# Kernel optimization log

Measured on AMD Instinct MI355X. Metric: run time of the kernel, lower is better.

Reference implementation:

```python
import jax, jax.numpy as jnp
import numpy as np

NUM_GROUPS = 32
EPS = 1e-6


def group_norm(x, gamma, beta):
    b, c, h, w = x.shape
    xg = x.reshape(b, NUM_GROUPS, c // NUM_GROUPS, h, w)
    mean = jnp.mean(xg, axis=(2, 3, 4), keepdims=True)
    var = jnp.var(xg, axis=(2, 3, 4), keepdims=True)
    xg = (xg - mean) * jax.lax.rsqrt(var + EPS)
    x = xg.reshape(b, c, h, w)
    return x * gamma[None, :, None, None] + beta[None, :, None, None]


def conv1x1(x, w, b):
    # x: [B,C,H,W], w: [Cout,Cin], b: [Cout]
    return jnp.einsum('bchw,oc->bohw', x, w) + b[None, :, None, None]


def setup_inputs() -> dict:
    key = jax.random.key(0)
    ks = jax.random.split(key, 11)
    B, C, H, W = 2, 512, 64, 64
    s = 1.0 / np.sqrt(C)
    return {
        'x': jax.random.normal(ks[0], (B, C, H, W), jnp.float32),
        'norm_gamma': jnp.ones((C,), jnp.float32),
        'norm_beta': jnp.zeros((C,), jnp.float32),
        'wq': jax.random.normal(ks[1], (C, C), jnp.float32) * s,
        'bq': jnp.zeros((C,), jnp.float32),
        'wk': jax.random.normal(ks[2], (C, C), jnp.float32) * s,
        'bk': jnp.zeros((C,), jnp.float32),
        'wv': jax.random.normal(ks[3], (C, C), jnp.float32) * s,
        'bv': jnp.zeros((C,), jnp.float32),
        'wo': jax.random.normal(ks[4], (C, C), jnp.float32) * s,
        'bo': jnp.zeros((C,), jnp.float32),
    }


def reference(x, norm_gamma, norm_beta, wq, bq, wk, bk, wv, bv, wo, bo):
    b, c, h, w = x.shape
    hn = group_norm(x, norm_gamma, norm_beta)
    q = conv1x1(hn, wq, bq).reshape(b, c, h * w)  # [B,C,HW]
    k = conv1x1(hn, wk, bk).reshape(b, c, h * w)
    v = conv1x1(hn, wv, bv).reshape(b, c, h * w)
    scale = jnp.asarray(c, x.dtype) ** -0.5
    # scores[b,i,j] = sum_c q[b,c,i] * k[b,c,j]
    scores = jnp.einsum('bci,bcj->bij', q, k) * scale
    attn = jax.nn.softmax(scores, axis=2)
    # out[b,c,i] = sum_j v[b,c,j] * attn[b,i,j]
    out = jnp.einsum('bcj,bij->bci', v, attn).reshape(b, c, h, w)
    out = conv1x1(out, wo, bo)
    return x + out
```

## Files before the change

### kernel.cpp

```cpp
#include <hip/hip_runtime.h>
#include <hip/hip_bf16.h>

using u16 = unsigned short;
typedef __attribute__((ext_vector_type(4))) float f32x4;
typedef __attribute__((ext_vector_type(8))) __bf16 bf16x8;
typedef __attribute__((ext_vector_type(8))) short s16x8;
typedef __attribute__((ext_vector_type(4))) short s16x4;

#define DEVI __device__ __forceinline__

constexpr int BATCH = 2, C = 512, HW = 4096, NG = 32, CPG = 16;

DEVI float b2f(u16 u) { union { unsigned u; float f; } a; a.u = ((unsigned)u) << 16; return a.f; }
DEVI u16 f2b(float f) {
  union { float f; unsigned u; } a; a.f = f;
  unsigned r = a.u + 0x7fffu + ((a.u >> 16) & 1u);
  return (u16)(r >> 16);
}

DEVI void xcd_remap(int& bx, int& by, int& bz) {
  const int nx = gridDim.x, ny = gridDim.y;
  const int nwg = nx * ny * gridDim.z;
  const int flat = blockIdx.x + nx * (blockIdx.y + ny * blockIdx.z);
  const int cpx = nwg >> 3;
  const int w = (flat & 7) * cpx + (flat >> 3);
  bx = w % nx;
  const int t = w / nx;
  by = t % ny;
  bz = t / ny;
}

__global__ __launch_bounds__(256) void cvt_w(const float* __restrict__ a, const float* __restrict__ b,
                                             const float* __restrict__ c, const float* __restrict__ d,
                                             u16* __restrict__ out, float* __restrict__ stats) {
  if (blockIdx.x == 0 && threadIdx.x < 128) stats[threadIdx.x] = 0.f;
  int i = blockIdx.x * 256 + threadIdx.x;
  int w = i >> 16;
  int off = (i & 65535) * 4;
  const float* s = (w == 0) ? a : (w == 1) ? b : (w == 2) ? c : d;
  f32x4 v = *(const f32x4*)(s + off);
  s16x4 o;
  o[0] = (short)f2b(v[0]); o[1] = (short)f2b(v[1]); o[2] = (short)f2b(v[2]); o[3] = (short)f2b(v[3]);
  *(s16x4*)(out + (size_t)w * 262144 + off) = o;
}

__global__ __launch_bounds__(256) void gn_stats(const float* __restrict__ x, float* __restrict__ stats) {
  const int bg = blockIdx.x >> 3, part = blockIdx.x & 7;
  const f32x4* xg = (const f32x4*)(x + (size_t)bg * (CPG * HW)) + part * 2048;
  float s = 0.f, ss = 0.f;
  #pragma unroll
  for (int i = 0; i < 8; ++i) {
    f32x4 v = xg[i * 256 + threadIdx.x];
    s += v[0] + v[1] + v[2] + v[3];
    ss += v[0] * v[0] + v[1] * v[1] + v[2] * v[2] + v[3] * v[3];
  }
  #pragma unroll
  for (int o = 32; o; o >>= 1) { s += __shfl_xor(s, o); ss += __shfl_xor(ss, o); }
  if ((threadIdx.x & 63) == 0) {
    atomicAdd(&stats[bg * 2], s);
    atomicAdd(&stats[bg * 2 + 1], ss);
  }
}

__global__ __launch_bounds__(256) void gn_normT(const float* __restrict__ x, const float* __restrict__ stats,
                                                const float* __restrict__ gamma, const float* __restrict__ beta,
                                                u16* __restrict__ hnT) {
  __shared__ u16 tile[64][66];
  int b = blockIdx.z, c0 = blockIdx.y * 64, h0 = blockIdx.x * 64;
  int t = threadIdx.x;
  const float* xb = x + ((size_t)b * C + c0) * HW + h0;
  int r = t / 16, cc = (t % 16) * 4;
  const float inv = 1.f / (float)(CPG * HW);
  #pragma unroll
  for (int it = 0; it < 4; ++it) {
    int rr = it * 16 + r;
    int ch = c0 + rr;
    int g = b * NG + (ch >> 4);
    float S = stats[g * 2], SS = stats[g * 2 + 1];
    float mean = S * inv;
    float rstd = rsqrtf(SS * inv - mean * mean + 1e-6f);
    float ga = gamma[ch] * rstd;
    float be = beta[ch] - mean * ga;
    f32x4 v = *(const f32x4*)(xb + (size_t)rr * HW + cc);
    #pragma unroll
    for (int j = 0; j < 4; ++j) tile[rr][cc + j] = f2b(v[j] * ga + be);
  }
  __syncthreads();
  u16* op = hnT + (size_t)b * HW * C + (size_t)h0 * C + c0;
  int hr2 = t / 8, cg = (t % 8) * 8;
  #pragma unroll
  for (int it = 0; it < 2; ++it) {
    int hr = it * 32 + hr2;
    s16x8 o8;
    #pragma unroll
    for (int j = 0; j < 8; ++j) o8[j] = (short)tile[cg + j][hr];
    *(s16x8*)(op + (size_t)hr * C + cg) = o8;
  }
}

#define EPI_BIAS_M 1
#define EPI_BIAS_N 2
#define EPI_RESID  4
#define EPI_F32OUT 8
#define EPI_QK     32

template <int EPI>
__global__ __launch_bounds__(256) void gemm_bt(const u16* __restrict__ A, const u16* __restrict__ Bt,
                                               void* __restrict__ Co, int M, int N, int K,
                                               long long sA, long long sB, long long sC,
                                               const float* __restrict__ bias,
                                               const float* __restrict__ biasB,
                                               const float* __restrict__ resid, long long sR) {
  (void)M;
  __shared__ u16 ldsA[128 * 64];
  __shared__ u16 ldsB[128 * 64];
  const int tid = threadIdx.x;
  int bn, bm, bz;
  xcd_remap(bn, bm, bz);
  A += (size_t)bz * sA;
  Bt += (size_t)bz * sB;
  const int wave = tid >> 6, lane = tid & 63;
  const int wr = wave >> 1, wc = wave & 1;
  f32x4 acc[4][4] = {};

  const int srow = tid >> 3;
  const int sch = (tid & 7) ^ (srow & 7);
  const u16* gA = A + (size_t)(bm * 128 + srow) * K + sch * 8;
  const u16* gB = Bt + (size_t)(bn * 128 + srow) * K + sch * 8;
  u16* lA = ldsA + wave * 512;
  u16* lB = ldsB + wave * 512;

  for (int k0 = 0; k0 < K; k0 += 64) {
    #pragma unroll
    for (int cc = 0; cc < 4; ++cc) {
      __builtin_amdgcn_global_load_lds(
          (const __attribute__((address_space(1))) void*)(gA + (size_t)cc * 32 * K + k0),
          (__attribute__((address_space(3))) void*)(lA + cc * 2048), 16, 0, 0);
      __builtin_amdgcn_global_load_lds(
          (const __attribute__((address_space(1))) void*)(gB + (size_t)cc * 32 * K + k0),
          (__attribute__((address_space(3))) void*)(lB + cc * 2048), 16, 0, 0);
    }
    __syncthreads();
    #pragma unroll
    for (int kk = 0; kk < 2; ++kk) {
      bf16x8 af[4], bfv[4];
      #pragma unroll
      for (int m = 0; m < 4; ++m) {
        int r = wr * 64 + m * 16 + (lane & 15);
        int chunk = (kk * 4 + (lane >> 4)) ^ (r & 7);
        af[m] = *(const bf16x8*)(ldsA + r * 64 + chunk * 8);
      }
      #pragma unroll
      for (int n = 0; n < 4; ++n) {
        int r = wc * 64 + n * 16 + (lane & 15);
        int chunk = (kk * 4 + (lane >> 4)) ^ (r & 7);
        bfv[n] = *(const bf16x8*)(ldsB + r * 64 + chunk * 8);
      }
      #pragma unroll
      for (int m = 0; m < 4; ++m)
        #pragma unroll
        for (int n = 0; n < 4; ++n)
          acc[m][n] = __builtin_amdgcn_mfma_f32_16x16x32_bf16(af[m], bfv[n], acc[m][n], 0, 0, 0);
    }
    __syncthreads();
  }

  const int col0 = bn * 128 + wc * 64;
  const int row0 = bm * 128 + wr * 64 + ((lane >> 4) << 2);
  #pragma unroll
  for (int m = 0; m < 4; ++m) {
    #pragma unroll
    for (int j = 0; j < 4; ++j) {
      int gm = row0 + m * 16 + j;
      float bm_v = (EPI & EPI_BIAS_M) ? bias[gm] : 0.f;
      #pragma unroll
      for (int n = 0; n < 4; ++n) {
        int gn = col0 + n * 16 + (lane & 15);
        float v = acc[m][n][j] + bm_v;
        if (EPI & EPI_BIAS_N) {
          if (EPI & EPI_QK) v += (gn < 512) ? bias[gn] : biasB[gn - 512];
          else v += bias[gn];
        }
        if (EPI & EPI_RESID) v += resid[(size_t)bz * sR + (size_t)gm * N + gn];
        if (EPI & EPI_F32OUT)
          ((float*)Co)[(size_t)bz * sC + (size_t)gm * N + gn] = v;
        else
          ((u16*)Co)[(size_t)bz * sC + (size_t)gm * N + gn] = f2b(v);
      }
    }
  }
}

template <bool SCALED>
__global__ __launch_bounds__(512, 2) void gemm256(
    const u16* __restrict__ Ag, const u16* __restrict__ Bg,
    u16* __restrict__ Co, u16* __restrict__ Co2, int zSwitch,
    int Nld, int ldK, int nsplitLog, int kLen,
    long long sA, long long sB, long long sC, float scale) {
  __shared__ u16 lds[65536];
  const int tid = threadIdx.x;
  const int lane = tid & 63, w = tid >> 6;
  const int wm = w >> 2, wn = w & 3;
  const int l15 = lane & 15, l4 = lane >> 4;
  int bn, bm, z;
  xcd_remap(bn, bm, z);
  const int bz = z >> nsplitLog, kz = z & ((1 << nsplitLog) - 1);
  const int kStart = kz * kLen;
  const int NT = kLen >> 6;

  const int rStage = w * 8 + (lane >> 3);
  const int gch = (lane & 7) ^ (lane >> 3);
  const u16* gA = Ag + (size_t)bz * sA + (size_t)(bm * 256) * ldK + kStart + gch * 8;
  const u16* gB = Bg + (size_t)bz * sB + (size_t)(bn * 256) * ldK + kStart + gch * 8;

  f32x4 acc[8][4] = {};
  bf16x8 aF[4][2], bF[2][2][2];

  const int hB = wn >> 1, qB = wn & 1;
  const u16* pA0 = lds + (0 * 4 + wm) * 8192;
  const u16* pA1 = lds + (1 * 4 + wm) * 8192;
  const u16* pB0 = lds + (0 * 4 + 2 + hB) * 8192;
  const u16* pB1 = lds + (1 * 4 + 2 + hB) * 8192;

  #define STAGE(TT, DB, AB, HF) { \
    const u16* gbase = (AB) ? gB : gA; \
    u16* l0 = lds + ((DB) * 4 + (AB) * 2 + (HF)) * 8192 + w * 512; \
    _Pragma("unroll") for (int s = 0; s < 2; ++s) { \
      const u16* gp = gbase + (size_t)((HF) * 128 + s * 64 + rStage) * ldK + (TT) * 64; \
      __builtin_amdgcn_global_load_lds((const __attribute__((address_space(1))) void*)gp, \
          (__attribute__((address_space(3))) void*)(l0 + s * 4096), 16, 0, 0); } }

  #define LOAD_A(P, MH) { _Pragma("unroll") for (int j = 0; j < 4; ++j) \
    _Pragma("unroll") for (int kk = 0; kk < 2; ++kk) { \
      const int r_ = (MH) * 64 + j * 16 + l15; const int c_ = (kk * 4 + l4) ^ (r_ & 7); \
      aF[j][kk] = *(const bf16x8*)((P) + r_ * 64 + c_ * 8); } }

  #define LOAD_B(P, NH) { _Pragma("unroll") for (int j = 0; j < 2; ++j) \
    _Pragma("unroll") for (int kk = 0; kk < 2; ++kk) { \
      const int r_ = qB * 64 + (NH) * 32 + j * 16 + l15; const int c_ = (kk * 4 + l4) ^ (r_ & 7); \
      bF[NH][j][kk] = *(const bf16x8*)((P) + r_ * 64 + c_ * 8); } }

  #define MM(MH, NH) { __builtin_amdgcn_s_setprio(1); \
    _Pragma("unroll") for (int j = 0; j < 4; ++j) \
      _Pragma("unroll") for (int j2 = 0; j2 < 2; ++j2) \
        _Pragma("unroll") for (int kk = 0; kk < 2; ++kk) \
          acc[(MH) * 4 + j][(NH) * 2 + j2] = __builtin_amdgcn_mfma_f32_16x16x32_bf16( \
              aF[j][kk], bF[NH][j2][kk], acc[(MH) * 4 + j][(NH) * 2 + j2], 0, 0, 0); \
    __builtin_amdgcn_s_setprio(0); }

  #define BAR __builtin_amdgcn_s_barrier()
  #define WLG { asm volatile("s_waitcnt lgkmcnt(0)" ::: "memory"); __builtin_amdgcn_sched_barrier(0); }
  #define LG8 asm volatile("s_waitcnt lgkmcnt(8)" ::: "memory")
  #define WV4 asm volatile("s_waitcnt vmcnt(4)" ::: "memory")
  #define WV0 asm volatile("s_waitcnt vmcnt(0)" ::: "memory")

  STAGE(0, 0, 1, 0); STAGE(0, 0, 1, 1);
  STAGE(0, 0, 0, 0); STAGE(0, 0, 0, 1);
  STAGE(1, 1, 1, 0); STAGE(1, 1, 1, 1);
  WV4; BAR;

  const int NI = NT / 2 - 1;
  for (int i = 0; i < NI; ++i) {
    const int t1 = 2 * i + 1, u0 = 2 * i + 2, u1 = 2 * i + 3;
    LOAD_A(pA0, 0); LOAD_B(pB0, 0); STAGE(t1, 1, 0, 0); LG8; BAR; WLG; MM(0, 0); BAR;
    LOAD_B(pB0, 1); STAGE(t1, 1, 0, 1); BAR; WLG; MM(0, 1); BAR;
    LOAD_A(pA0, 1); STAGE(u0, 0, 1, 0); BAR; WLG; MM(1, 1); BAR;
    STAGE(u0, 0, 1, 1); BAR; WLG; MM(1, 0); WV4; BAR;
    LOAD_A(pA1, 0); LOAD_B(pB1, 0); STAGE(u0, 0, 0, 0); LG8; BAR; WLG; MM(0, 0); BAR;
    LOAD_B(pB1, 1); STAGE(u0, 0, 0, 1); BAR; WLG; MM(0, 1); BAR;
    LOAD_A(pA1, 1); STAGE(u1, 1, 1, 0); BAR; WLG; MM(1, 1); BAR;
    STAGE(u1, 1, 1, 1); BAR; WLG; MM(1, 0); WV4; BAR;
  }
  {
    const int t1 = NT - 1;
    LOAD_A(pA0, 0); LOAD_B(pB0, 0); STAGE(t1, 1, 0, 0); LG8; BAR; WLG; MM(0, 0); BAR;
    LOAD_B(pB0, 1); STAGE(t1, 1, 0, 1); BAR; WLG; MM(0, 1); BAR;
    LOAD_A(pA0, 1); BAR; WLG; MM(1, 1); BAR;
    BAR; WLG; MM(1, 0); WV0; BAR;
    LOAD_A(pA1, 0); LOAD_B(pB1, 0); LG8; BAR; WLG; MM(0, 0); BAR;
    LOAD_B(pB1, 1); BAR; WLG; MM(0, 1); BAR;
    LOAD_A(pA1, 1); BAR; WLG; MM(1, 1); BAR;
    MM(1, 0);
  }
  #undef STAGE
  #undef LOAD_A
  #undef LOAD_B
  #undef MM
  #undef BAR
  #undef WLG
  #undef LG8
  #undef WV4
  #undef WV0

  __syncthreads();
  {
    const int rloc = wm * 128 + l4 * 4;
    const int cloc = wn * 64 + l15;
    #pragma unroll
    for (int m = 0; m < 8; ++m) {
      #pragma unroll
      for (int j = 0; j < 4; ++j) {
        const int r_ = rloc + m * 16 + j;
        const int xr = ((r_ >> 2) & 3) << 5;
        #pragma unroll
        for (int n = 0; n < 4; ++n) {
          float v = acc[m][n][j];
          if (SCALED) v *= scale;
          *(u16*)((char*)lds + ((r_ * 512 + (cloc + n * 16) * 2) ^ xr)) = f2b(v);
        }
      }
    }
    __syncthreads();
    u16* outp = (z < zSwitch) ? (Co + (size_t)z * sC) : (Co2 + (size_t)(z - zSwitch) * sC);
    #pragma unroll
    for (int it = 0; it < 16; ++it) {
      const int idx = it * 512 + tid;
      const int r_ = idx >> 5, ch = idx & 31;
      const int xr = ((r_ >> 2) & 3) << 5;
      s16x8 d8 = *(const s16x8*)((const char*)lds + ((r_ * 512 + ch * 16) ^ xr));
      *(s16x8*)(outp + (size_t)(bm * 256 + r_) * Nld + bn * 256 + ch * 8) = d8;
    }
  }
}

__global__ __launch_bounds__(256) void softmax_rows(u16* __restrict__ S) {
  int row = blockIdx.x * 4 + (threadIdx.x >> 6);
  int lane = threadIdx.x & 63;
  s16x8* p = (s16x8*)(S + (size_t)row * 4096);
  float v[64];
  float m = -1e30f;
  #pragma unroll
  for (int j = 0; j < 8; ++j) {
    s16x8 raw = p[j * 64 + lane];
    #pragma unroll
    for (int e = 0; e < 8; ++e) {
      float f = b2f((u16)raw[e]);
      v[j * 8 + e] = f;
      m = fmaxf(m, f);
    }
  }
  #pragma unroll
  for (int o = 32; o; o >>= 1) m = fmaxf(m, __shfl_xor(m, o));
  float s = 0.f;
  #pragma unroll
  for (int i = 0; i < 64; ++i) { v[i] = __expf(v[i] - m); s += v[i]; }
  #pragma unroll
  for (int o = 32; o; o >>= 1) s += __shfl_xor(s, o);
  float r = 1.f / s;
  #pragma unroll
  for (int j = 0; j < 8; ++j) {
    s16x8 o8;
    #pragma unroll
    for (int e = 0; e < 8; ++e) o8[e] = (short)f2b(v[j * 8 + e] * r);
    p[j * 64 + lane] = o8;
  }
}

__global__ __launch_bounds__(256) void reduce_pv(const u16* __restrict__ P, const u16* __restrict__ P2,
                                                 u16* __restrict__ ao) {
  const size_t e = ((size_t)blockIdx.x * 256 + threadIdx.x) * 8;
  const int b = (int)(e >> 21);
  const size_t o = e & 2097151;
  float s[8] = {0.f, 0.f, 0.f, 0.f, 0.f, 0.f, 0.f, 0.f};
  #pragma unroll
  for (int kz = 0; kz < 4; ++kz) {
    const int zz = b * 4 + kz;
    const u16* src = (zz < 6) ? (P + (size_t)zz * 2097152) : (P2 + (size_t)(zz - 6) * 2097152);
    s16x8 v = *(const s16x8*)(src + o);
    #pragma unroll
    for (int j = 0; j < 8; ++j) s[j] += b2f((u16)v[j]);
  }
  s16x8 o8;
  #pragma unroll
  for (int j = 0; j < 8; ++j) o8[j] = (short)f2b(s[j]);
  *(s16x8*)(ao + e) = o8;
}

extern "C" void kernel_launch(void* const* d_in, const int* in_sizes, int n_in,
                              void* d_out, int out_size, void* d_ws, size_t ws_size,
                              hipStream_t stream) {
  (void)in_sizes; (void)n_in; (void)out_size; (void)ws_size;
  const float* x     = (const float*)d_in[0];
  const float* gamma = (const float*)d_in[1];
  const float* beta  = (const float*)d_in[2];
  const float* wq    = (const float*)d_in[3];
  const float* bq    = (const float*)d_in[4];
  const float* wk    = (const float*)d_in[5];
  const float* bk    = (const float*)d_in[6];
  const float* wv    = (const float*)d_in[7];
  const float* bv    = (const float*)d_in[8];
  const float* wo    = (const float*)d_in[9];
  const float* bo    = (const float*)d_in[10];

  char* ws = (char*)d_ws;
  const size_t MiB = 1024 * 1024;
  float* stats = (float*)ws;
  u16* wbf = (u16*)(ws + 1024);
  u16* vv  = (u16*)(ws + 4 * MiB);
  u16* qkT = (u16*)(ws + 12 * MiB);
  u16* hnT = (u16*)(ws + 28 * MiB);
  u16* Ppart = (u16*)(ws + 12 * MiB);
  u16* Sm  = (u16*)(ws + 36 * MiB);
  u16* aoT = (u16*)(ws + 36 * MiB);

  const long long sTok  = (long long)HW * C;
  const long long sTok2 = (long long)HW * 1024;
  const long long sS    = (long long)HW * HW;
  const float scale = 0.044194173824159216f;

  cvt_w<<<dim3(1024), dim3(256), 0, stream>>>(wq, wk, wv, wo, wbf, stats);
  gn_stats<<<dim3(512), dim3(256), 0, stream>>>(x, stats);
  gn_normT<<<dim3(HW / 64, C / 64, BATCH), dim3(256), 0, stream>>>(x, stats, gamma, beta, hnT);

  gemm_bt<EPI_BIAS_N | EPI_QK><<<dim3(8, 32, BATCH), dim3(256), 0, stream>>>(
      hnT, wbf, qkT, HW, 1024, C, sTok, 0, sTok2, bq, bk, nullptr, 0);
  gemm_bt<EPI_BIAS_M><<<dim3(32, 4, BATCH), dim3(256), 0, stream>>>(
      wbf + 2 * 262144, hnT, vv, C, HW, C, 0, sTok, sTok, bv, nullptr, nullptr, 0);

  gemm256<true><<<dim3(16, 16, BATCH), dim3(512), 0, stream>>>(
      qkT, qkT + 512, Sm, Sm, 1000, HW, 1024, 0, C, sTok2, sTok2, sS, scale);

  softmax_rows<<<dim3(2048), dim3(256), 0, stream>>>(Sm);

  gemm256<false><<<dim3(2, 16, BATCH * 4), dim3(512), 0, stream>>>(
      Sm, vv, Ppart, (u16*)d_out, 6, C, HW, 2, HW / 4, sS, sTok, (long long)2097152, 1.f);

  reduce_pv<<<dim3(2048), dim3(256), 0, stream>>>(Ppart, (const u16*)d_out, aoT);

  gemm_bt<EPI_BIAS_M | EPI_RESID | EPI_F32OUT><<<dim3(32, 4, BATCH), dim3(256), 0, stream>>>(
      wbf + 3 * 262144, aoT, d_out, C, HW, C, 0, sTok, (long long)C * HW, bo, nullptr, x, (long long)C * HW);
}
```

Measured before the change: 185.9 us.

## Fuse softmax exponentiation into PV GEMM and defer normalization to reduce

The softmax kernel now only computes each row's max and reciprocal sum and no longer rewrites the 4096x4096 score matrix. The PV GEMM stages raw scores into an extra LDS region and applies exp(s - max) while copying them into the swizzled operand buffer. The 1/sum normalization moves into the split-K reduction. This removes a full read-modify-write pass over the score matrix, at the cost of extra LDS, exp work and a synchronous transform step inside the GEMM pipeline, which could reduce occupancy and overlap.

After: 190.7 us. 1.03x slower.

```diff
diff --git a/kernel.cpp b/kernel.cpp
--- a/kernel.cpp
+++ b/kernel.cpp
@@ -191,13 +191,15 @@
   }
 }
 
-template <bool SCALED>
+template <bool SCALED, bool FUSEEXP>
 __global__ __launch_bounds__(512, 2) void gemm256(
     const u16* __restrict__ Ag, const u16* __restrict__ Bg,
     u16* __restrict__ Co, u16* __restrict__ Co2, int zSwitch,
     int Nld, int ldK, int nsplitLog, int kLen,
-    long long sA, long long sB, long long sC, float scale) {
-  __shared__ u16 lds[65536];
+    long long sA, long long sB, long long sC, float scale,
+    const float* __restrict__ mrowp) {
+  constexpr int LDSE = FUSEEXP ? 81920 : 65536;
+  __shared__ u16 lds[LDSE];
   const int tid = threadIdx.x;
   const int lane = tid & 63, w = tid >> 6;
   const int wm = w >> 2, wn = w & 3;
@@ -210,8 +212,18 @@
 
   const int rStage = w * 8 + (lane >> 3);
   const int gch = (lane & 7) ^ (lane >> 3);
-  const u16* gA = Ag + (size_t)bz * sA + (size_t)(bm * 256) * ldK + kStart + gch * 8;
+  const u16* gA = Ag + (size_t)bz * sA + (size_t)(bm * 256) * ldK + kStart +
+                  (FUSEEXP ? (lane & 7) * 8 : gch * 8);
   const u16* gB = Bg + (size_t)bz * sB + (size_t)(bn * 256) * ldK + kStart + gch * 8;
+
+  float mv[4] = {0.f, 0.f, 0.f, 0.f};
+  if (FUSEEXP) {
+    #pragma unroll
+    for (int hf = 0; hf < 2; ++hf)
+      #pragma unroll
+      for (int s2 = 0; s2 < 2; ++s2)
+        mv[hf * 2 + s2] = mrowp[(size_t)bz * 4096 + bm * 256 + hf * 128 + s2 * 64 + rStage];
+  }
 
   f32x4 acc[8][4] = {};
   bf16x8 aF[4][2], bF[2][2][2];
@@ -222,13 +234,33 @@
   const u16* pB0 = lds + (0 * 4 + 2 + hB) * 8192;
   const u16* pB1 = lds + (1 * 4 + 2 + hB) * 8192;
 
-  #define STAGE(TT, DB, AB, HF) { \
-    const u16* gbase = (AB) ? gB : gA; \
-    u16* l0 = lds + ((DB) * 4 + (AB) * 2 + (HF)) * 8192 + w * 512; \
-    _Pragma("unroll") for (int s = 0; s < 2; ++s) { \
-      const u16* gp = gbase + (size_t)((HF) * 128 + s * 64 + rStage) * ldK + (TT) * 64; \
+  #define STAGEB(TT, DB, HF) { \
+    u16* l0 = lds + ((DB) * 4 + 2 + (HF)) * 8192 + w * 512; \
+    _Pragma("unroll") for (int s2 = 0; s2 < 2; ++s2) { \
+      const u16* gp = gB + (size_t)((HF) * 128 + s2 * 64 + rStage) * ldK + (TT) * 64; \
       __builtin_amdgcn_global_load_lds((const __attribute__((address_space(1))) void*)gp, \
-          (__attribute__((address_space(3))) void*)(l0 + s * 4096), 16, 0, 0); } }
+          (__attribute__((address_space(3))) void*)(l0 + s2 * 4096), 16, 0, 0); } }
+
+  #define STAGEA(TT, DB, HF) { \
+    u16* l0 = FUSEEXP ? (lds + 65536 + (HF) * 8192 + w * 512) \
+                      : (lds + ((DB) * 4 + (HF)) * 8192 + w * 512); \
+    _Pragma("unroll") for (int s2 = 0; s2 < 2; ++s2) { \
+      const u16* gp = gA + (size_t)((HF) * 128 + s2 * 64 + rStage) * ldK + (TT) * 64; \
+      __builtin_amdgcn_global_load_lds((const __attribute__((address_space(1))) void*)gp, \
+          (__attribute__((address_space(3))) void*)(l0 + s2 * 4096), 16, 0, 0); } }
+
+  #define TRANSFORM(DB) { if (FUSEEXP) { \
+    _Pragma("unroll") for (int hf = 0; hf < 2; ++hf) \
+      _Pragma("unroll") for (int s2 = 0; s2 < 2; ++s2) { \
+        s16x8 raw = *(const s16x8*)(lds + 65536 + hf * 8192 + s2 * 4096 + w * 512 + lane * 8); \
+        const float mrw = mv[hf * 2 + s2]; \
+        s16x8 ov; \
+        _Pragma("unroll") for (int e = 0; e < 8; ++e) \
+          ov[e] = (short)f2b(__expf(b2f((u16)raw[e]) - mrw)); \
+        *(s16x8*)(lds + ((DB) * 4 + hf) * 8192 + (s2 * 64 + rStage) * 64 + \
+                  (((lane & 7) ^ (rStage & 7)) * 8)) = ov; } \
+    asm volatile("s_waitcnt lgkmcnt(0)" ::: "memory"); \
+    __builtin_amdgcn_sched_barrier(0); } }
 
   #define LOAD_A(P, MH) { _Pragma("unroll") for (int j = 0; j < 4; ++j) \
     _Pragma("unroll") for (int kk = 0; kk < 2; ++kk) { \
@@ -250,45 +282,45 @@
 
   #define BAR __builtin_amdgcn_s_barrier()
   #define WLG { asm volatile("s_waitcnt lgkmcnt(0)" ::: "memory"); __builtin_amdgcn_sched_barrier(0); }
-  #define LG8 asm volatile("s_waitcnt lgkmcnt(8)" ::: "memory")
   #define WV4 asm volatile("s_waitcnt vmcnt(4)" ::: "memory")
   #define WV0 asm volatile("s_waitcnt vmcnt(0)" ::: "memory")
 
-  STAGE(0, 0, 1, 0); STAGE(0, 0, 1, 1);
-  STAGE(0, 0, 0, 0); STAGE(0, 0, 0, 1);
-  STAGE(1, 1, 1, 0); STAGE(1, 1, 1, 1);
-  WV4; BAR;
+  STAGEB(0, 0, 0); STAGEB(0, 0, 1);
+  STAGEA(0, 0, 0); STAGEA(0, 0, 1);
+  STAGEB(1, 1, 0); STAGEB(1, 1, 1);
+  WV4; TRANSFORM(0); BAR;
 
   const int NI = NT / 2 - 1;
   for (int i = 0; i < NI; ++i) {
     const int t1 = 2 * i + 1, u0 = 2 * i + 2, u1 = 2 * i + 3;
-    LOAD_A(pA0, 0); LOAD_B(pB0, 0); STAGE(t1, 1, 0, 0); LG8; BAR; WLG; MM(0, 0); BAR;
-    LOAD_B(pB0, 1); STAGE(t1, 1, 0, 1); BAR; WLG; MM(0, 1); BAR;
-    LOAD_A(pA0, 1); STAGE(u0, 0, 1, 0); BAR; WLG; MM(1, 1); BAR;
-    STAGE(u0, 0, 1, 1); BAR; WLG; MM(1, 0); WV4; BAR;
-    LOAD_A(pA1, 0); LOAD_B(pB1, 0); STAGE(u0, 0, 0, 0); LG8; BAR; WLG; MM(0, 0); BAR;
-    LOAD_B(pB1, 1); STAGE(u0, 0, 0, 1); BAR; WLG; MM(0, 1); BAR;
-    LOAD_A(pA1, 1); STAGE(u1, 1, 1, 0); BAR; WLG; MM(1, 1); BAR;
-    STAGE(u1, 1, 1, 1); BAR; WLG; MM(1, 0); WV4; BAR;
+    LOAD_A(pA0, 0); LOAD_B(pB0, 0); STAGEA(t1, 1, 0); BAR; WLG; MM(0, 0); BAR;
+    LOAD_B(pB0, 1); STAGEA(t1, 1, 1); BAR; WLG; MM(0, 1); BAR;
+    LOAD_A(pA0, 1); STAGEB(u0, 0, 0); BAR; WLG; MM(1, 1); BAR;
+    STAGEB(u0, 0, 1); BAR; WLG; MM(1, 0); WV4; TRANSFORM(1); BAR;
+    LOAD_A(pA1, 0); LOAD_B(pB1, 0); STAGEA(u0, 0, 0); BAR; WLG; MM(0, 0); BAR;
+    LOAD_B(pB1, 1); STAGEA(u0, 0, 1); BAR; WLG; MM(0, 1); BAR;
+    LOAD_A(pA1, 1); STAGEB(u1, 1, 0); BAR; WLG; MM(1, 1); BAR;
+    STAGEB(u1, 1, 1); BAR; WLG; MM(1, 0); WV4; TRANSFORM(0); BAR;
   }
   {
     const int t1 = NT - 1;
-    LOAD_A(pA0, 0); LOAD_B(pB0, 0); STAGE(t1, 1, 0, 0); LG8; BAR; WLG; MM(0, 0); BAR;
-    LOAD_B(pB0, 1); STAGE(t1, 1, 0, 1); BAR; WLG; MM(0, 1); BAR;
+    LOAD_A(pA0, 0); LOAD_B(pB0, 0); STAGEA(t1, 1, 0); BAR; WLG; MM(0, 0); BAR;
+    LOAD_B(pB0, 1); STAGEA(t1, 1, 1); BAR; WLG; MM(0, 1); BAR;
     LOAD_A(pA0, 1); BAR; WLG; MM(1, 1); BAR;
-    BAR; WLG; MM(1, 0); WV0; BAR;
-    LOAD_A(pA1, 0); LOAD_B(pB1, 0); LG8; BAR; WLG; MM(0, 0); BAR;
+    BAR; WLG; MM(1, 0); WV0; TRANSFORM(1); BAR;
+    LOAD_A(pA1, 0); LOAD_B(pB1, 0); BAR; WLG; MM(0, 0); BAR;
     LOAD_B(pB1, 1); BAR; WLG; MM(0, 1); BAR;
     LOAD_A(pA1, 1); BAR; WLG; MM(1, 1); BAR;
     MM(1, 0);
   }
-  #undef STAGE
+  #undef STAGEB
+  #undef STAGEA
+  #undef TRANSFORM
   #undef LOAD_A
   #undef LOAD_B
   #undef MM
   #undef BAR
   #undef WLG
-  #undef LG8
   #undef WV4
   #undef WV0
 
@@ -323,10 +355,11 @@
   }
 }
 
-__global__ __launch_bounds__(256) void softmax_rows(u16* __restrict__ S) {
+__global__ __launch_bounds__(256) void rowstats(const u16* __restrict__ S,
+                                                float* __restrict__ mrow, float* __restrict__ rinv) {
   int row = blockIdx.x * 4 + (threadIdx.x >> 6);
   int lane = threadIdx.x & 63;
-  s16x8* p = (s16x8*)(S + (size_t)row * 4096);
+  const s16x8* p = (const s16x8*)(S + (size_t)row * 4096);
   float v[64];
   float m = -1e30f;
   #pragma unroll
@@ -343,24 +376,22 @@
   for (int o = 32; o; o >>= 1) m = fmaxf(m, __shfl_xor(m, o));
   float s = 0.f;
   #pragma unroll
-  for (int i = 0; i < 64; ++i) { v[i] = __expf(v[i] - m); s += v[i]; }
+  for (int i = 0; i < 64; ++i) s += __expf(v[i] - m);
   #pragma unroll
   for (int o = 32; o; o >>= 1) s += __shfl_xor(s, o);
-  float r = 1.f / s;
-  #pragma unroll
-  for (int j = 0; j < 8; ++j) {
-    s16x8 o8;
-    #pragma unroll
-    for (int e = 0; e < 8; ++e) o8[e] = (short)f2b(v[j * 8 + e] * r);
-    p[j * 64 + lane] = o8;
+  if (lane == 0) {
+    mrow[row] = m;
+    rinv[row] = 1.f / s;
   }
 }
 
 __global__ __launch_bounds__(256) void reduce_pv(const u16* __restrict__ P, const u16* __restrict__ P2,
-                                                 u16* __restrict__ ao) {
+                                                 const float* __restrict__ rinv, u16* __restrict__ ao) {
   const size_t e = ((size_t)blockIdx.x * 256 + threadIdx.x) * 8;
   const int b = (int)(e >> 21);
   const size_t o = e & 2097151;
+  const int row = (int)(o >> 9);
+  const float rv = rinv[(size_t)b * 4096 + row];
   float s[8] = {0.f, 0.f, 0.f, 0.f, 0.f, 0.f, 0.f, 0.f};
   #pragma unroll
   for (int kz = 0; kz < 4; ++kz) {
@@ -372,7 +403,7 @@
   }
   s16x8 o8;
   #pragma unroll
-  for (int j = 0; j < 8; ++j) o8[j] = (short)f2b(s[j]);
+  for (int j = 0; j < 8; ++j) o8[j] = (short)f2b(s[j] * rv);
   *(s16x8*)(ao + e) = o8;
 }
 
@@ -396,6 +427,8 @@
   const size_t MiB = 1024 * 1024;
   float* stats = (float*)ws;
   u16* wbf = (u16*)(ws + 1024);
+  float* mrow = (float*)(ws + 3 * MiB);
+  float* rinv = (float*)(ws + 3 * MiB + 32768);
   u16* vv  = (u16*)(ws + 4 * MiB);
   u16* qkT = (u16*)(ws + 12 * MiB);
   u16* hnT = (u16*)(ws + 28 * MiB);
@@ -417,15 +450,15 @@
   gemm_bt<EPI_BIAS_M><<<dim3(32, 4, BATCH), dim3(256), 0, stream>>>(
       wbf + 2 * 262144, hnT, vv, C, HW, C, 0, sTok, sTok, bv, nullptr, nullptr, 0);
 
-  gemm256<true><<<dim3(16, 16, BATCH), dim3(512), 0, stream>>>(
-      qkT, qkT + 512, Sm, Sm, 1000, HW, 1024, 0, C, sTok2, sTok2, sS, scale);
-
-  softmax_rows<<<dim3(2048), dim3(256), 0, stream>>>(Sm);
-
-  gemm256<false><<<dim3(2, 16, BATCH * 4), dim3(512), 0, stream>>>(
-      Sm, vv, Ppart, (u16*)d_out, 6, C, HW, 2, HW / 4, sS, sTok, (long long)2097152, 1.f);
-
-  reduce_pv<<<dim3(2048), dim3(256), 0, stream>>>(Ppart, (const u16*)d_out, aoT);
+  gemm256<true, false><<<dim3(16, 16, BATCH), dim3(512), 0, stream>>>(
+      qkT, qkT + 512, Sm, Sm, 1000, HW, 1024, 0, C, sTok2, sTok2, sS, scale, nullptr);
+
+  rowstats<<<dim3(2048), dim3(256), 0, stream>>>(Sm, mrow, rinv);
+
+  gemm256<false, true><<<dim3(2, 16, BATCH * 4), dim3(512), 0, stream>>>(
+      Sm, vv, Ppart, (u16*)d_out, 6, C, HW, 2, HW / 4, sS, sTok, (long long)2097152, 1.f, mrow);
+
+  reduce_pv<<<dim3(2048), dim3(256), 0, stream>>>(Ppart, (const u16*)d_out, rinv, aoT);
 
   gemm_bt<EPI_BIAS_M | EPI_RESID | EPI_F32OUT><<<dim3(32, 4, BATCH), dim3(256), 0, stream>>>(
       wbf + 3 * 262144, aoT, d_out, C, HW, C, 0, sTok, (long long)C * HW, bo, nullptr, x, (long long)C * HW);
```
